# Kernel optimization log

Measured on AMD Instinct MI355X. Metric: run time of the kernel, lower is better.

Reference implementation:

```python
import jax, jax.numpy as jnp
import numpy as np


def setup_inputs() -> dict:
    key = jax.random.key(0)
    ks = jax.random.split(key, 10)
    B, D_X, D_H, D_S, D_T = 16384, 256, 512, 128, 128
    G = 4 * D_H
    sc = lambda d: 1.0 / np.sqrt(d)
    return {
        "x": jax.random.normal(ks[0], (B, D_X), jnp.float32),
        "h": jax.random.normal(ks[1], (B, D_H), jnp.float32),
        "c": jax.random.normal(ks[2], (B, D_H), jnp.float32),
        "spatial_per_step": jax.random.normal(ks[3], (B, D_S), jnp.float32),
        "temporal_per_step": jax.random.normal(ks[4], (B, D_T), jnp.float32),
        "W_x": jax.random.normal(ks[5], (D_X, G), jnp.float32) * sc(D_X),
        "W_h": jax.random.normal(ks[6], (D_H, G), jnp.float32) * sc(D_H),
        "b_h": jax.random.normal(ks[7], (G,), jnp.float32) * 0.01,
        "W_s": jax.random.normal(ks[8], (D_S, G), jnp.float32) * sc(D_S),
        "W_t": jax.random.normal(ks[9], (D_T, G), jnp.float32) * sc(D_T),
    }


def reference(x, h, c, spatial_per_step, temporal_per_step, W_x, W_h, b_h, W_s, W_t):
    H = W_h.shape[0]  # hidden_size
    # Four gate projections summed (the fusion opportunity): [B, 4H]
    preact = (x @ W_x) + (h @ W_h + b_h) + (spatial_per_step @ W_s) + (temporal_per_step @ W_t)
    i_g = jax.nn.sigmoid(preact[:, 0 * H:1 * H])
    f_g = jax.nn.sigmoid(preact[:, 1 * H:2 * H])
    o_g = jax.nn.sigmoid(preact[:, 2 * H:3 * H])
    c_g = jnp.tanh(preact[:, 3 * H:4 * H])
    c_new = f_g * c + i_g * c_g
    # NOTE: faithful to the source, h = tanh(o * c) (not o * tanh(c))
    h_new = jnp.tanh(o_g * c_new)
    return (h_new, c_new)
```

## Files before the change

kernel.cpp:

```cpp
#include <hip/hip_runtime.h>
#include <hip/hip_bf16.h>
#include <cstdint>

#define B_DIM 16384
#define DX 256
#define DH 512
#define DS 128
#define DT 128
#define KDIM 1024
#define NDIM 2048
#define HOUT 512

typedef __attribute__((ext_vector_type(8))) short short8;
typedef __attribute__((ext_vector_type(4))) float floatx4;

union bf16x8 {
  short8 v;
  __hip_bfloat16 b[8];
};

__device__ __forceinline__ float fast_sigmoid(float x) {
  return 1.f / (1.f + __expf(-x));
}
__device__ __forceinline__ float fast_tanh(float x) {
  float e = __expf(-2.f * x);
  return (1.f - e) / (1.f + e);
}


__global__ __launch_bounds__(256) void pack_A(
    const float* __restrict__ x, const float* __restrict__ h,
    const float* __restrict__ s, const float* __restrict__ t,
    __hip_bfloat16* __restrict__ Ap) {
  int tid = blockIdx.x * 256 + threadIdx.x;
  int i = tid & 63;
  int tt = (tid >> 6) & 15;
  int tile = tid >> 10;
  int kb = tile & 15, mb = tile >> 4;
  int sp = tt >> 3, c = tt & 7;
  int b = mb * 128 + c * 16 + (i >> 2);
  int k = kb * 64 + sp * 32 + (i & 3) * 8;
  const float* p;
  if (k < 256)      p = x + (size_t)b * DX + k;
  else if (k < 768) p = h + (size_t)b * DH + (k - 256);
  else if (k < 896) p = s + (size_t)b * DS + (k - 768);
  else              p = t + (size_t)b * DT + (k - 896);
  floatx4 v0 = *(const floatx4*)p;
  floatx4 v1 = *(const floatx4*)(p + 4);
  bf16x8 o;
#pragma unroll
  for (int j = 0; j < 4; ++j) {
    o.b[j]     = __float2bfloat16(v0[j]);
    o.b[4 + j] = __float2bfloat16(v1[j]);
  }
  *(short8*)(Ap + (size_t)tid * 8) = o.v;
}

__global__ __launch_bounds__(256) void pack_W(
    const float* __restrict__ Wx, const float* __restrict__ Wh,
    const float* __restrict__ Ws, const float* __restrict__ Wt,
    __hip_bfloat16* __restrict__ Wp) {
  int tid = blockIdx.x * 256 + threadIdx.x;
  int i = tid & 63;
  int tt = (tid >> 6) & 15;
  int tile = tid >> 10;
  int kb = tile & 15, nblk = tile >> 4;
  int sp = tt >> 3, c = tt & 7;
  int nl = c * 16 + (i >> 2);
  int k = kb * 64 + sp * 32 + (i & 3) * 8;
  int wn = nl >> 6, g = (nl >> 4) & 3, hl = nl & 15;
  int col = g * 512 + nblk * 32 + wn * 16 + hl;
  const float* src; int kl;
  if (k < 256)      { src = Wx; kl = k; }
  else if (k < 768) { src = Wh; kl = k - 256; }
  else if (k < 896) { src = Ws; kl = k - 768; }
  else              { src = Wt; kl = k - 896; }
  bf16x8 o;
#pragma unroll
  for (int r = 0; r < 8; ++r)
    o.b[r] = __float2bfloat16(src[(size_t)(kl + r) * NDIM + col]);
  *(short8*)(Wp + (size_t)tid * 8) = o.v;
}

__global__ __launch_bounds__(256, 3) void lstm_gemm(
    const __hip_bfloat16* __restrict__ Ap, const __hip_bfloat16* __restrict__ Wp,
    const float* __restrict__ bh, const float* __restrict__ c_in,
    float* __restrict__ out) {
  __shared__ unsigned short As[2 * 128 * 32];

  const int tid = threadIdx.x;
  const int lane = tid & 63;
  const int wid = tid >> 6;
  const int wm = wid & 1;
  const int wn = wid >> 1;
  const int q = lane >> 4;
  const int fr = lane & 15;
  const int mb = blockIdx.y;
  const int nblk = blockIdx.x;
  const int m0 = mb * 128;

  floatx4 acc[4][4];
#pragma unroll
  for (int i = 0; i < 4; ++i)
#pragma unroll
    for (int j = 0; j < 4; ++j) acc[i][j] = (floatx4)0.f;

  const int blane = (fr * 4 + q) * 8;

  for (int kt = 0; kt < KDIM / 64; ++kt) {
    const size_t abase = ((size_t)(mb * 16 + kt) * 16) * 512;
#pragma unroll
    for (int j = 0; j < 4; ++j) {
      const int chunk = wid * 4 + j;
      __builtin_amdgcn_global_load_lds(
          (const __attribute__((address_space(1))) void*)
              (Ap + abase + (size_t)chunk * 512 + lane * 8),
          (__attribute__((address_space(3))) void*)&As[chunk * 512], 16, 0, 0);
    }
    short8 bf[2][4];
    const size_t bbase = ((size_t)(nblk * 16 + kt) * 16) * 512;
#pragma unroll
    for (int sp = 0; sp < 2; ++sp)
#pragma unroll
      for (int ni = 0; ni < 4; ++ni)
        bf[sp][ni] = *(const short8*)(Wp + bbase +
                         (size_t)(sp * 8 + wn * 4 + ni) * 512 + blane);
    __syncthreads();

#pragma unroll
    for (int sp = 0; sp < 2; ++sp) {
      short8 af[4];
#pragma unroll
      for (int mi = 0; mi < 4; ++mi)
        af[mi] = *(const short8*)&As[sp * 4096 +
                                     (wm * 64 + mi * 16 + fr) * 32 + q * 8];
#pragma unroll
      for (int mi = 0; mi < 4; ++mi)
#pragma unroll
        for (int ni = 0; ni < 4; ++ni)
          acc[mi][ni] = __builtin_amdgcn_mfma_f32_16x16x32_bf16(
              af[mi], bf[sp][ni], acc[mi][ni], 0, 0, 0);
    }
    __syncthreads();
  }

  const int hh = nblk * 32 + wn * 16 + fr;
  float bias[4];
#pragma unroll
  for (int g = 0; g < 4; ++g) bias[g] = bh[g * 512 + hh];

#pragma unroll
  for (int mi = 0; mi < 4; ++mi) {
#pragma unroll
    for (int r = 0; r < 4; ++r) {
      const size_t grow = (size_t)(m0 + wm * 64 + mi * 16 + q * 4 + r);
      const float pi = acc[mi][0][r] + bias[0];
      const float pf = acc[mi][1][r] + bias[1];
      const float po = acc[mi][2][r] + bias[2];
      const float pc = acc[mi][3][r] + bias[3];
      const float ig = fast_sigmoid(pi);
      const float fg = fast_sigmoid(pf);
      const float og = fast_sigmoid(po);
      const float cg = fast_tanh(pc);
      const float cc = fg * c_in[grow * HOUT + hh] + ig * cg;
      out[grow * HOUT + hh] = fast_tanh(og * cc);
      out[(size_t)B_DIM * HOUT + grow * HOUT + hh] = cc;
    }
  }
}

extern "C" void kernel_launch(void* const* d_in, const int* in_sizes, int n_in,
                              void* d_out, int out_size, void* d_ws, size_t ws_size,
                              hipStream_t stream) {
  const float* x  = (const float*)d_in[0];
  const float* h  = (const float*)d_in[1];
  const float* c  = (const float*)d_in[2];
  const float* sp = (const float*)d_in[3];
  const float* tp = (const float*)d_in[4];
  const float* Wx = (const float*)d_in[5];
  const float* Wh = (const float*)d_in[6];
  const float* bh = (const float*)d_in[7];
  const float* Ws = (const float*)d_in[8];
  const float* Wt = (const float*)d_in[9];
  float* out = (float*)d_out;

  __hip_bfloat16* Ap = (__hip_bfloat16*)d_ws;
  __hip_bfloat16* Wp = (__hip_bfloat16*)((char*)d_ws + (size_t)B_DIM * KDIM * 2);

  pack_A<<<dim3(B_DIM * KDIM / 8 / 256), dim3(256), 0, stream>>>(x, h, sp, tp, Ap);
  pack_W<<<dim3(NDIM * KDIM / 8 / 256), dim3(256), 0, stream>>>(Wx, Wh, Ws, Wt, Wp);
  lstm_gemm<<<dim3(NDIM / 128, B_DIM / 128), dim3(256), 0, stream>>>(Ap, Wp, bh, c, out);
}
```

Measured before the change: 251.4 us.

## Stage B tiles through LDS with direct loads and halve K step

The weight operand now goes global→LDS through global_load_lds, the same way A already does, instead of per-wave register loads from global memory. This removes the duplicated B fetch across the two M-waves. The K step per iteration drops from 64 to 32, so each iteration moves smaller A and B tiles, and the launch-bounds occupancy hint rises from 3 to 4 blocks. The cost is twice as many loop iterations and barrier pairs with no double buffering, which exposes load latency more often.

```diff
diff --git a/kernel.cpp b/kernel.cpp
--- a/kernel.cpp
+++ b/kernel.cpp
@@ -82,11 +82,12 @@
   *(short8*)(Wp + (size_t)tid * 8) = o.v;
 }
 
-__global__ __launch_bounds__(256, 3) void lstm_gemm(
+__global__ __launch_bounds__(256, 4) void lstm_gemm(
     const __hip_bfloat16* __restrict__ Ap, const __hip_bfloat16* __restrict__ Wp,
     const float* __restrict__ bh, const float* __restrict__ c_in,
     float* __restrict__ out) {
-  __shared__ unsigned short As[2 * 128 * 32];
+  __shared__ unsigned short As[128 * 32];
+  __shared__ unsigned short Bs[128 * 32];
 
   const int tid = threadIdx.x;
   const int lane = tid & 63;
@@ -105,42 +106,35 @@
 #pragma unroll
     for (int j = 0; j < 4; ++j) acc[i][j] = (floatx4)0.f;
 
-  const int blane = (fr * 4 + q) * 8;
-
-  for (int kt = 0; kt < KDIM / 64; ++kt) {
-    const size_t abase = ((size_t)(mb * 16 + kt) * 16) * 512;
+  for (int p = 0; p < 32; ++p) {
+    const size_t abase = ((size_t)((mb * 16 + (p >> 1)) * 16 + (p & 1) * 8)) * 512;
+    const size_t bbase = ((size_t)((nblk * 16 + (p >> 1)) * 16 + (p & 1) * 8)) * 512;
 #pragma unroll
-    for (int j = 0; j < 4; ++j) {
-      const int chunk = wid * 4 + j;
+    for (int j = 0; j < 2; ++j) {
+      const int chunk = wid * 2 + j;
       __builtin_amdgcn_global_load_lds(
           (const __attribute__((address_space(1))) void*)
               (Ap + abase + (size_t)chunk * 512 + lane * 8),
           (__attribute__((address_space(3))) void*)&As[chunk * 512], 16, 0, 0);
+      __builtin_amdgcn_global_load_lds(
+          (const __attribute__((address_space(1))) void*)
+              (Wp + bbase + (size_t)chunk * 512 + lane * 8),
+          (__attribute__((address_space(3))) void*)&Bs[chunk * 512], 16, 0, 0);
     }
-    short8 bf[2][4];
-    const size_t bbase = ((size_t)(nblk * 16 + kt) * 16) * 512;
+    __syncthreads();
+
+    short8 af[4], bf[4];
 #pragma unroll
-    for (int sp = 0; sp < 2; ++sp)
+    for (int i = 0; i < 4; ++i) {
+      af[i] = *(const short8*)&As[(wm * 64 + i * 16 + fr) * 32 + q * 8];
+      bf[i] = *(const short8*)&Bs[(wn * 64 + i * 16 + fr) * 32 + q * 8];
+    }
+#pragma unroll
+    for (int mi = 0; mi < 4; ++mi)
 #pragma unroll
       for (int ni = 0; ni < 4; ++ni)
-        bf[sp][ni] = *(const short8*)(Wp + bbase +
-                         (size_t)(sp * 8 + wn * 4 + ni) * 512 + blane);
-    __syncthreads();
-
-#pragma unroll
-    for (int sp = 0; sp < 2; ++sp) {
-      short8 af[4];
-#pragma unroll
-      for (int mi = 0; mi < 4; ++mi)
-        af[mi] = *(const short8*)&As[sp * 4096 +
-                                     (wm * 64 + mi * 16 + fr) * 32 + q * 8];
-#pragma unroll
-      for (int mi = 0; mi < 4; ++mi)
-#pragma unroll
-        for (int ni = 0; ni < 4; ++ni)
-          acc[mi][ni] = __builtin_amdgcn_mfma_f32_16x16x32_bf16(
-              af[mi], bf[sp][ni], acc[mi][ni], 0, 0, 0);
-    }
+        acc[mi][ni] = __builtin_amdgcn_mfma_f32_16x16x32_bf16(
+            af[mi], bf[ni], acc[mi][ni], 0, 0, 0);
     __syncthreads();
   }
 
```

New measurement: 242.6 us. 3.5% less time.
